# Kernel optimization log

Hardware: AMD Instinct MI355X
Metric: run time of the kernel (lower is better)

Reference implementation:

```python
import jax, jax.numpy as jnp
import numpy as np

S, C1, C2, N = 4096, 2048, 2048, 1024


def setup_inputs() -> dict:
    key = jax.random.key(0)
    k1, k2, k3, k4 = jax.random.split(key, 4)
    # child log-likelihoods (samples, child_nodes); modest scale so exp() stays finite,
    # matching the (numerically naive) torch forward which exps without max-subtraction.
    ll1 = jax.random.normal(k1, (S, C1), dtype=jnp.float32)
    ll2 = jax.random.normal(k2, (S, C2), dtype=jnp.float32)
    # log edge weights, one tensor per child layer: (nodes, child_nodes)
    w1 = jax.random.normal(k3, (N, C1), dtype=jnp.float32)
    w2 = jax.random.normal(k4, (N, C2), dtype=jnp.float32)
    return {"ll1": ll1, "ll2": ll2, "w1": w1, "w2": w2}


def reference(ll1, ll2, w1, w2):
    # Per child layer: sum_c exp(ll[s,c] + w[n,c]) == exp(ll) @ exp(w).T  -> (S, N)
    # (same math as unsqueeze/repeat/exp/sum in the torch code, without the (S,C,N) blowup)
    result = jnp.exp(ll1) @ jnp.exp(w1).T + jnp.exp(ll2) @ jnp.exp(w2).T  # (S, N)
    # per-node log normalization constant over concatenated weights
    log_z = jax.nn.logsumexp(jnp.concatenate([w1, w2], axis=1), axis=1)  # (N,)
    return jnp.log(result) - log_z[None, :]
```

## Files before the change

### kernel.cpp

```cpp
#include <hip/hip_runtime.h>

#define S_DIM 4096
#define C_DIM 2048
#define N_DIM 1024
#define K_DIM 4096

#define BM 64
#define BN 128
#define BK 32
#define NT (K_DIM / BK)
#define TILE_BYTES 12288
#define NBUF 3

typedef __attribute__((ext_vector_type(8))) short bf16x8;
typedef __attribute__((ext_vector_type(4))) float f32x4;

__device__ static inline unsigned short f2bf(float f) {
    unsigned int u = __float_as_uint(f);
    u += 0x7FFFu + ((u >> 16) & 1u);
    return (unsigned short)(u >> 16);
}

__global__ void exp_ll_kernel(const float* __restrict__ ll1,
                              const float* __restrict__ ll2,
                              unsigned short* __restrict__ A) {
    const int total4 = S_DIM * C_DIM / 4;
    int stride = gridDim.x * blockDim.x;
    for (int i = blockIdx.x * blockDim.x + threadIdx.x; i < total4; i += stride) {
        int e = i << 2;
        int r = e >> 11;
        int c = e & 2047;
        size_t dst = ((size_t)r << 12) + c;
        float4 v = *reinterpret_cast<const float4*>(ll1 + e);
        ushort4 o;
        o.x = f2bf(__expf(v.x)); o.y = f2bf(__expf(v.y));
        o.z = f2bf(__expf(v.z)); o.w = f2bf(__expf(v.w));
        *reinterpret_cast<ushort4*>(A + dst) = o;
        float4 u = *reinterpret_cast<const float4*>(ll2 + e);
        ushort4 p;
        p.x = f2bf(__expf(u.x)); p.y = f2bf(__expf(u.y));
        p.z = f2bf(__expf(u.z)); p.w = f2bf(__expf(u.w));
        *reinterpret_cast<ushort4*>(A + dst + C_DIM) = p;
    }
}

__global__ void w_kernel(const float* __restrict__ w1,
                         const float* __restrict__ w2,
                         unsigned short* __restrict__ B,
                         float* __restrict__ lz) {
    const int n = blockIdx.x;
    const int tid = threadIdx.x;
    const int lane = tid & 63, wv = tid >> 6;
    const float* r1 = w1 + ((size_t)n << 11);
    const float* r2 = w2 + ((size_t)n << 11);
    float4 v0 = *reinterpret_cast<const float4*>(r1 + tid * 8);
    float4 v1 = *reinterpret_cast<const float4*>(r1 + tid * 8 + 4);
    float4 u0 = *reinterpret_cast<const float4*>(r2 + tid * 8);
    float4 u1 = *reinterpret_cast<const float4*>(r2 + tid * 8 + 4);

    float mx = fmaxf(fmaxf(fmaxf(v0.x, v0.y), fmaxf(v0.z, v0.w)),
                     fmaxf(fmaxf(v1.x, v1.y), fmaxf(v1.z, v1.w)));
    mx = fmaxf(mx, fmaxf(fmaxf(fmaxf(u0.x, u0.y), fmaxf(u0.z, u0.w)),
                          fmaxf(fmaxf(u1.x, u1.y), fmaxf(u1.z, u1.w))));
    #pragma unroll
    for (int off = 32; off > 0; off >>= 1) mx = fmaxf(mx, __shfl_xor(mx, off));
    __shared__ float red[4];
    if (lane == 0) red[wv] = mx;
    __syncthreads();
    mx = fmaxf(fmaxf(red[0], red[1]), fmaxf(red[2], red[3]));

    float s = __expf(v0.x - mx) + __expf(v0.y - mx) + __expf(v0.z - mx) + __expf(v0.w - mx)
            + __expf(v1.x - mx) + __expf(v1.y - mx) + __expf(v1.z - mx) + __expf(v1.w - mx)
            + __expf(u0.x - mx) + __expf(u0.y - mx) + __expf(u0.z - mx) + __expf(u0.w - mx)
            + __expf(u1.x - mx) + __expf(u1.y - mx) + __expf(u1.z - mx) + __expf(u1.w - mx);
    #pragma unroll
    for (int off = 32; off > 0; off >>= 1) s += __shfl_xor(s, off);
    __shared__ float red2[4];
    if (lane == 0) red2[wv] = s;
    __syncthreads();
    if (tid == 0)
        lz[n] = mx + __logf(red2[0] + red2[1] + red2[2] + red2[3]);

    unsigned short* brow = B + ((size_t)n << 12);
    ushort4 o;
    o.x = f2bf(__expf(v0.x)); o.y = f2bf(__expf(v0.y));
    o.z = f2bf(__expf(v0.z)); o.w = f2bf(__expf(v0.w));
    *reinterpret_cast<ushort4*>(brow + tid * 8) = o;
    o.x = f2bf(__expf(v1.x)); o.y = f2bf(__expf(v1.y));
    o.z = f2bf(__expf(v1.z)); o.w = f2bf(__expf(v1.w));
    *reinterpret_cast<ushort4*>(brow + tid * 8 + 4) = o;
    o.x = f2bf(__expf(u0.x)); o.y = f2bf(__expf(u0.y));
    o.z = f2bf(__expf(u0.z)); o.w = f2bf(__expf(u0.w));
    *reinterpret_cast<ushort4*>(brow + C_DIM + tid * 8) = o;
    o.x = f2bf(__expf(u1.x)); o.y = f2bf(__expf(u1.y));
    o.z = f2bf(__expf(u1.z)); o.w = f2bf(__expf(u1.w));
    *reinterpret_cast<ushort4*>(brow + C_DIM + tid * 8 + 4) = o;
}

typedef const unsigned int __attribute__((address_space(1)))* gas_ptr;
typedef unsigned int __attribute__((address_space(3)))* las_ptr;

__global__ __launch_bounds__(256) void gemm_log_kernel(
        const unsigned short* __restrict__ A,
        const unsigned short* __restrict__ B,
        const float* __restrict__ lz,
        float* __restrict__ out) {
    __shared__ __align__(16) char lds[NBUF * TILE_BYTES];
    const int tid  = threadIdx.x;
    const int l    = tid & 63;
    const int w    = tid >> 6;
    const int bn = blockIdx.x & 7;
    const int bm = blockIdx.x >> 3;
    const int wr = w & 1, wc = w >> 1;
    const int lcol = l & 15, lk = l >> 4;

    const int kg = (l & 3) ^ ((l >> 3) & 3);
    const unsigned short* src[3];
    int dst[3];
    #pragma unroll
    for (int g = 0; g < 3; ++g) {
        const int row = g * 64 + w * 16 + (l >> 2);
        src[g] = (g == 0)
            ? A + (size_t)(bm * BM + row) * K_DIM + kg * 8
            : B + (size_t)(bn * BN + row - 64) * K_DIM + kg * 8;
        dst[g] = row * 64 + (l & 3) * 16;
    }

    const int swz = (lk ^ ((lcol >> 1) & 3)) << 4;
    int aoff[2], boff[4];
    #pragma unroll
    for (int m = 0; m < 2; ++m) aoff[m] = (wr * 32 + m * 16 + lcol) * 64 + swz;
    #pragma unroll
    for (int n = 0; n < 4; ++n) boff[n] = 4096 + (wc * 64 + n * 16 + lcol) * 64 + swz;

    f32x4 acc[2][4] = {};

#define GLOAD(p, o) __builtin_amdgcn_global_load_lds((gas_ptr)(const void*)(p), \
        (las_ptr)(void*)(lds + (o)), 16, 0, 0)
#define STAGE(T, BUFB) { const int _ko = (T) * BK; const int _bo = (BUFB) * TILE_BYTES; \
        GLOAD(src[0] + _ko, _bo + dst[0]); GLOAD(src[1] + _ko, _bo + dst[1]);           \
        GLOAD(src[2] + _ko, _bo + dst[2]); }
#define BODY(T, BUF, BUFS, WAITN, DOSTAGE) {                                            \
        asm volatile("s_waitcnt vmcnt(" #WAITN ")" ::: "memory");                       \
        __builtin_amdgcn_s_barrier();                                                   \
        if (DOSTAGE) STAGE((T) + 2, BUFS);                                              \
        const char* base = lds + (BUF) * TILE_BYTES;                                    \
        bf16x8 a[2], b[4];                                                              \
        _Pragma("unroll") for (int m = 0; m < 2; ++m)                                   \
            a[m] = *reinterpret_cast<const bf16x8*>(base + aoff[m]);                    \
        _Pragma("unroll") for (int n = 0; n < 4; ++n)                                   \
            b[n] = *reinterpret_cast<const bf16x8*>(base + boff[n]);                    \
        _Pragma("unroll") for (int m = 0; m < 2; ++m)                                   \
            _Pragma("unroll") for (int n = 0; n < 4; ++n)                               \
                acc[m][n] = __builtin_amdgcn_mfma_f32_16x16x32_bf16(a[m], b[n],         \
                                                                   acc[m][n], 0, 0, 0); }

    STAGE(0, 0);
    STAGE(1, 1);
    for (int t3 = 0; t3 < NT - 2; t3 += 3) {
        BODY(t3 + 0, 0, 2, 3, 1);
        BODY(t3 + 1, 1, 0, 3, 1);
        BODY(t3 + 2, 2, 1, 3, 1);
    }
    BODY(NT - 2, 0, 2, 3, 0);
    BODY(NT - 1, 1, 0, 0, 0);
#undef BODY
#undef STAGE
#undef GLOAD

    const int col_base = bn * BN + wc * 64;
    float lzv[4];
    #pragma unroll
    for (int n = 0; n < 4; ++n) lzv[n] = lz[col_base + n * 16 + lcol];
    #pragma unroll
    for (int m = 0; m < 2; ++m) {
        const int row0 = bm * BM + wr * 32 + m * 16 + lk * 4;
        #pragma unroll
        for (int n = 0; n < 4; ++n) {
            const int col = col_base + n * 16 + lcol;
            #pragma unroll
            for (int j = 0; j < 4; ++j)
                out[(size_t)(row0 + j) * N_DIM + col] = __logf(acc[m][n][j]) - lzv[n];
        }
    }
}

__global__ void naive_kernel(const float* __restrict__ ll1, const float* __restrict__ ll2,
                             const float* __restrict__ w1, const float* __restrict__ w2,
                             float* __restrict__ out) {
    int idx = blockIdx.x * blockDim.x + threadIdx.x;
    if (idx >= S_DIM * N_DIM) return;
    int s = idx >> 10, n = idx & (N_DIM - 1);
    const float* a1 = ll1 + (size_t)s * C_DIM;
    const float* a2 = ll2 + (size_t)s * C_DIM;
    const float* b1 = w1 + (size_t)n * C_DIM;
    const float* b2 = w2 + (size_t)n * C_DIM;
    float mx = -3.0e38f;
    for (int c = 0; c < C_DIM; ++c) mx = fmaxf(mx, b1[c]);
    for (int c = 0; c < C_DIM; ++c) mx = fmaxf(mx, b2[c]);
    float zs = 0.f, acc = 0.f;
    for (int c = 0; c < C_DIM; ++c) { zs += __expf(b1[c] - mx); acc += __expf(a1[c] + b1[c]); }
    for (int c = 0; c < C_DIM; ++c) { zs += __expf(b2[c] - mx); acc += __expf(a2[c] + b2[c]); }
    out[idx] = __logf(acc) - (mx + __logf(zs));
}

extern "C" void kernel_launch(void* const* d_in, const int* in_sizes, int n_in,
                              void* d_out, int out_size, void* d_ws, size_t ws_size,
                              hipStream_t stream) {
    const float* ll1 = (const float*)d_in[0];
    const float* ll2 = (const float*)d_in[1];
    const float* w1  = (const float*)d_in[2];
    const float* w2  = (const float*)d_in[3];
    float* out = (float*)d_out;

    const size_t a_elems = (size_t)S_DIM * K_DIM;
    const size_t b_elems = (size_t)N_DIM * K_DIM;
    const size_t need = (a_elems + b_elems) * sizeof(unsigned short) + N_DIM * sizeof(float);
    if (ws_size < need) {
        naive_kernel<<<(S_DIM * N_DIM + 255) / 256, 256, 0, stream>>>(ll1, ll2, w1, w2, out);
        return;
    }
    unsigned short* Aws = (unsigned short*)d_ws;
    unsigned short* Bws = Aws + a_elems;
    float* lzws = (float*)(Bws + b_elems);

    exp_ll_kernel<<<2048, 256, 0, stream>>>(ll1, ll2, Aws);
    w_kernel<<<N_DIM, 256, 0, stream>>>(w1, w2, Bws, lzws);
    gemm_log_kernel<<<(S_DIM / BM) * (N_DIM / BN), 256, 0, stream>>>(Aws, Bws, lzws, out);
}
```

Before: 82.29 us.

## Enlarge GEMM tile to 128x128 with deeper 8-buffer LDS pipeline

```diff
diff --git a/kernel.cpp b/kernel.cpp
--- a/kernel.cpp
+++ b/kernel.cpp
@@ -5,12 +5,12 @@
 #define N_DIM 1024
 #define K_DIM 4096
 
-#define BM 64
+#define BM 128
 #define BN 128
 #define BK 32
 #define NT (K_DIM / BK)
-#define TILE_BYTES 12288
-#define NBUF 3
+#define TILE_BYTES 16384
+#define NBUF 8
 
 typedef __attribute__((ext_vector_type(8))) short bf16x8;
 typedef __attribute__((ext_vector_type(4))) float f32x4;
@@ -100,7 +100,7 @@
 typedef const unsigned int __attribute__((address_space(1)))* gas_ptr;
 typedef unsigned int __attribute__((address_space(3)))* las_ptr;
 
-__global__ __launch_bounds__(256) void gemm_log_kernel(
+__global__ __launch_bounds__(256, 1) void gemm_log_kernel(
         const unsigned short* __restrict__ A,
         const unsigned short* __restrict__ B,
         const float* __restrict__ lz,
@@ -111,59 +111,67 @@
     const int w    = tid >> 6;
     const int bn = blockIdx.x & 7;
     const int bm = blockIdx.x >> 3;
-    const int wr = w & 1, wc = w >> 1;
+    const int wr = w >> 1, wc = w & 1;
     const int lcol = l & 15, lk = l >> 4;
 
     const int kg = (l & 3) ^ ((l >> 3) & 3);
-    const unsigned short* src[3];
-    int dst[3];
-    #pragma unroll
-    for (int g = 0; g < 3; ++g) {
-        const int row = g * 64 + w * 16 + (l >> 2);
-        src[g] = (g == 0)
+    const unsigned short* src[4];
+    int dst[4];
+    #pragma unroll
+    for (int i = 0; i < 4; ++i) {
+        const int ri  = w * 4 + i;
+        const int row = ri * 16 + (l >> 2);
+        src[i] = (ri < 8)
             ? A + (size_t)(bm * BM + row) * K_DIM + kg * 8
-            : B + (size_t)(bn * BN + row - 64) * K_DIM + kg * 8;
-        dst[g] = row * 64 + (l & 3) * 16;
+            : B + (size_t)(bn * BN + row - 128) * K_DIM + kg * 8;
+        dst[i] = row * 64 + (l & 3) * 16;
     }
 
     const int swz = (lk ^ ((lcol >> 1) & 3)) << 4;
-    int aoff[2], boff[4];
-    #pragma unroll
-    for (int m = 0; m < 2; ++m) aoff[m] = (wr * 32 + m * 16 + lcol) * 64 + swz;
-    #pragma unroll
-    for (int n = 0; n < 4; ++n) boff[n] = 4096 + (wc * 64 + n * 16 + lcol) * 64 + swz;
-
-    f32x4 acc[2][4] = {};
+    int aoff[4], boff[4];
+    #pragma unroll
+    for (int m = 0; m < 4; ++m) aoff[m] = (wr * 64 + m * 16 + lcol) * 64 + swz;
+    #pragma unroll
+    for (int n = 0; n < 4; ++n) boff[n] = 8192 + (wc * 64 + n * 16 + lcol) * 64 + swz;
+
+    f32x4 acc[4][4] = {};
 
 #define GLOAD(p, o) __builtin_amdgcn_global_load_lds((gas_ptr)(const void*)(p), \
         (las_ptr)(void*)(lds + (o)), 16, 0, 0)
 #define STAGE(T, BUFB) { const int _ko = (T) * BK; const int _bo = (BUFB) * TILE_BYTES; \
         GLOAD(src[0] + _ko, _bo + dst[0]); GLOAD(src[1] + _ko, _bo + dst[1]);           \
-        GLOAD(src[2] + _ko, _bo + dst[2]); }
-#define BODY(T, BUF, BUFS, WAITN, DOSTAGE) {                                            \
+        GLOAD(src[2] + _ko, _bo + dst[2]); GLOAD(src[3] + _ko, _bo + dst[3]); }
+#define BODY(T, BUF, SBUF, WAITN, DOSTAGE) {                                            \
         asm volatile("s_waitcnt vmcnt(" #WAITN ")" ::: "memory");                       \
         __builtin_amdgcn_s_barrier();                                                   \
-        if (DOSTAGE) STAGE((T) + 2, BUFS);                                              \
+        if (DOSTAGE) STAGE((T) + 6, SBUF);                                              \
         const char* base = lds + (BUF) * TILE_BYTES;                                    \
-        bf16x8 a[2], b[4];                                                              \
-        _Pragma("unroll") for (int m = 0; m < 2; ++m)                                   \
+        bf16x8 a[4], b[4];                                                              \
+        _Pragma("unroll") for (int m = 0; m < 4; ++m)                                   \
             a[m] = *reinterpret_cast<const bf16x8*>(base + aoff[m]);                    \
         _Pragma("unroll") for (int n = 0; n < 4; ++n)                                   \
             b[n] = *reinterpret_cast<const bf16x8*>(base + boff[n]);                    \
-        _Pragma("unroll") for (int m = 0; m < 2; ++m)                                   \
+        _Pragma("unroll") for (int m = 0; m < 4; ++m)                                   \
             _Pragma("unroll") for (int n = 0; n < 4; ++n)                               \
                 acc[m][n] = __builtin_amdgcn_mfma_f32_16x16x32_bf16(a[m], b[n],         \
                                                                    acc[m][n], 0, 0, 0); }
 
-    STAGE(0, 0);
-    STAGE(1, 1);
-    for (int t3 = 0; t3 < NT - 2; t3 += 3) {
-        BODY(t3 + 0, 0, 2, 3, 1);
-        BODY(t3 + 1, 1, 0, 3, 1);
-        BODY(t3 + 2, 2, 1, 3, 1);
-    }
-    BODY(NT - 2, 0, 2, 3, 0);
-    BODY(NT - 1, 1, 0, 0, 0);
+    STAGE(0, 0); STAGE(1, 1); STAGE(2, 2);
+    STAGE(3, 3); STAGE(4, 4); STAGE(5, 5);
+    for (int t8 = 0; t8 < NT - 8; t8 += 8) {
+        BODY(t8 + 0, 0, 6, 20, 1); BODY(t8 + 1, 1, 7, 20, 1);
+        BODY(t8 + 2, 2, 0, 20, 1); BODY(t8 + 3, 3, 1, 20, 1);
+        BODY(t8 + 4, 4, 2, 20, 1); BODY(t8 + 5, 5, 3, 20, 1);
+        BODY(t8 + 6, 6, 4, 20, 1); BODY(t8 + 7, 7, 5, 20, 1);
+    }
+    BODY(NT - 8, 0, 6, 20, 1);
+    BODY(NT - 7, 1, 7, 20, 1);
+    BODY(NT - 6, 2, 0, 20, 0);
+    BODY(NT - 5, 3, 0, 16, 0);
+    BODY(NT - 4, 4, 0, 12, 0);
+    BODY(NT - 3, 5, 0,  8, 0);
+    BODY(NT - 2, 6, 0,  4, 0);
+    BODY(NT - 1, 7, 0,  0, 0);
 #undef BODY
 #undef STAGE
 #undef GLOAD
@@ -173,8 +181,8 @@
     #pragma unroll
     for (int n = 0; n < 4; ++n) lzv[n] = lz[col_base + n * 16 + lcol];
     #pragma unroll
-    for (int m = 0; m < 2; ++m) {
-        const int row0 = bm * BM + wr * 32 + m * 16 + lk * 4;
+    for (int m = 0; m < 4; ++m) {
+        const int row0 = bm * BM + wr * 64 + m * 16 + lk * 4;
         #pragma unroll
         for (int n = 0; n < 4; ++n) {
             const int col = col_base + n * 16 + lcol;
```

Result: faster. 70.85 us (-13.9%).
